# Optimization experiments

Measured on AMD Instinct MI355X. Metric: run time of the kernel, lower is better.

Reference implementation:

```python
import jax, jax.numpy as jnp
import numpy as np

N, E, F_IN, HID, HEADS, OUT = 50000, 800000, 128, 64, 4, 40


def gat_layer(x, src, dst, n, W, a_src, a_dst, b, heads, ch):
    # PyG GATConv: h = x @ W per head; e_ij = LeakyReLU(a_src.h_j + a_dst.h_i)
    h = (x @ W).reshape(n, heads, ch)
    al_s = jnp.einsum('nhc,hc->nh', h, a_src)  # source-side logit term
    al_d = jnp.einsum('nhc,hc->nh', h, a_dst)  # target-side logit term
    e = jax.nn.leaky_relu(al_s[src] + al_d[dst], negative_slope=0.2)  # [E,H]
    m = jax.ops.segment_max(e, dst, num_segments=n)  # stable softmax per target node
    e = jnp.exp(e - m[dst])
    s = jax.ops.segment_sum(e, dst, num_segments=n)
    alpha = e / s[dst]  # [E,H]
    out = jax.ops.segment_sum(h[src] * alpha[:, :, None], dst, num_segments=n)  # [n,H,C]
    return out.reshape(n, heads * ch) + b


def gat_forward(x, src, dst, W0, as0, ad0, b0, W1, as1, ad1, b1, W2, as2, ad2, b2):
    n = x.shape[0]
    x = jax.nn.elu(gat_layer(x, src, dst, n, W0, as0, ad0, b0, HEADS, HID))
    x = jax.nn.elu(gat_layer(x, src, dst, n, W1, as1, ad1, b1, HEADS, HID))
    x = gat_layer(x, src, dst, n, W2, as2, ad2, b2, 1, OUT)
    return jax.nn.log_softmax(x, axis=1)


def setup_inputs() -> dict:
    key = jax.random.key(0)
    ks = jax.random.split(key, 16)
    x = jax.random.normal(ks[0], (N, F_IN), dtype=jnp.float32)
    edge_index = jax.random.randint(ks[1], (2, E), 0, N, dtype=jnp.int64)
    g = lambda k, sh: jax.random.normal(k, sh, dtype=jnp.float32) * (1.0 / np.sqrt(sh[0]))
    d_hid = HID * HEADS
    return {
        'x': x, 'edge_index': edge_index,
        'W0': g(ks[2], (F_IN, d_hid)), 'as0': g(ks[3], (HEADS, HID)), 'ad0': g(ks[4], (HEADS, HID)), 'b0': jnp.zeros((d_hid,), jnp.float32),
        'W1': g(ks[5], (d_hid, d_hid)), 'as1': g(ks[6], (HEADS, HID)), 'ad1': g(ks[7], (HEADS, HID)), 'b1': jnp.zeros((d_hid,), jnp.float32),
        'W2': g(ks[8], (d_hid, OUT)), 'as2': g(ks[9], (1, OUT)), 'ad2': g(ks[10], (1, OUT)), 'b2': jnp.zeros((OUT,), jnp.float32),
    }


def reference(x, edge_index, W0, as0, ad0, b0, W1, as1, ad1, b1, W2, as2, ad2, b2):
    n = x.shape[0]
    loops = jnp.arange(n, dtype=edge_index.dtype)  # PyG add_self_loops=True
    src = jnp.concatenate([edge_index[0], loops])
    dst = jnp.concatenate([edge_index[1], loops])
    return gat_forward(x, src, dst, W0, as0, ad0, b0, W1, as1, ad1, b1, W2, as2, ad2, b2)
```

## Files before the change

kernel.cpp:

```cpp
#include <hip/hip_runtime.h>
#include <math.h>

#define NODES 50000
#define NEDGES 800000
#define TOT_E (NEDGES + NODES)
#define SCAN_B 256
#define SCAN_NB ((NODES + SCAN_B - 1) / SCAN_B)

typedef __attribute__((ext_vector_type(8))) short short8v;
typedef __attribute__((ext_vector_type(4))) float f32x4;

static __device__ __forceinline__ float lrelu(float z) {
  return z > 0.f ? z : 0.2f * z;
}
static __device__ __forceinline__ float b2f(ushort u) {
  union { uint i; float f; } v; v.i = ((uint)u) << 16; return v.f;
}
static __device__ __forceinline__ ushort f2b(float f) {
  union { float f; uint i; } v; v.f = f;
  uint r = v.i + 0x7fff + ((v.i >> 16) & 1);
  return (ushort)(r >> 16);
}

__global__ void k_hist(const int* __restrict__ dst, int* __restrict__ counts) {
  int stride = gridDim.x * blockDim.x;
  for (int i = blockIdx.x * blockDim.x + threadIdx.x; i < TOT_E; i += stride) {
    int d = (i < NEDGES) ? dst[i] : (i - NEDGES);
    atomicAdd(&counts[d], 1);
  }
}

__global__ __launch_bounds__(SCAN_B) void k_scan_red(const int* __restrict__ counts,
                                                     int* __restrict__ bsum) {
  __shared__ int sm[SCAN_B];
  int idx = blockIdx.x * SCAN_B + threadIdx.x;
  int v = (idx < NODES) ? counts[idx] : 0;
  sm[threadIdx.x] = v;
  __syncthreads();
  for (int off = SCAN_B / 2; off > 0; off >>= 1) {
    if (threadIdx.x < off) sm[threadIdx.x] += sm[threadIdx.x + off];
    __syncthreads();
  }
  if (threadIdx.x == 0) bsum[blockIdx.x] = sm[0];
}

__global__ __launch_bounds__(256) void k_scan_part(const int* __restrict__ bsum,
                                                   int* __restrict__ bpre) {
  __shared__ int sm[256];
  int tid = threadIdx.x;
  int v = (tid < SCAN_NB) ? bsum[tid] : 0;
  sm[tid] = v;
  __syncthreads();
  for (int off = 1; off < 256; off <<= 1) {
    int t = (tid >= off) ? sm[tid - off] : 0;
    __syncthreads();
    sm[tid] += t;
    __syncthreads();
  }
  if (tid < SCAN_NB) bpre[tid] = sm[tid] - v;
}

__global__ __launch_bounds__(SCAN_B) void k_scan_emit(const int* __restrict__ counts,
    const int* __restrict__ bpre, int* __restrict__ offs, int* __restrict__ cur) {
  __shared__ int sm[SCAN_B];
  int idx = blockIdx.x * SCAN_B + threadIdx.x;
  int tid = threadIdx.x;
  int v = (idx < NODES) ? counts[idx] : 0;
  sm[tid] = v;
  __syncthreads();
  for (int off = 1; off < SCAN_B; off <<= 1) {
    int t = (tid >= off) ? sm[tid - off] : 0;
    __syncthreads();
    sm[tid] += t;
    __syncthreads();
  }
  int base = bpre[blockIdx.x];
  int excl = base + sm[tid] - v;
  if (idx < NODES) { offs[idx] = excl; cur[idx] = excl; }
  if (idx == NODES - 1) offs[NODES] = excl + v;
}

__global__ void k_scatter(const int* __restrict__ src, const int* __restrict__ dst,
                          int* __restrict__ cur, int* __restrict__ ssrc) {
  int stride = gridDim.x * blockDim.x;
  for (int i = blockIdx.x * blockDim.x + threadIdx.x; i < TOT_E; i += stride) {
    int s, d;
    if (i < NEDGES) { s = src[i]; d = dst[i]; } else { s = i - NEDGES; d = s; }
    int pos = atomicAdd(&cur[d], 1);
    ssrc[pos] = s;
  }
}

__global__ void k_cast4(const float* __restrict__ X, ushort* __restrict__ Xb, int total4) {
  int stride = gridDim.x * blockDim.x;
  for (int i = blockIdx.x * blockDim.x + threadIdx.x; i < total4; i += stride) {
    float4 v = *(const float4*)&X[i * 4];
    ushort4 o;
    o.x = f2b(v.x); o.y = f2b(v.y); o.z = f2b(v.z); o.w = f2b(v.w);
    *(ushort4*)&Xb[i * 4] = o;
  }
}

__global__ void k_packB(const float* __restrict__ W, ushort* __restrict__ Bp,
                        int N, int NF, int total) {
  int idx = blockIdx.x * blockDim.x + threadIdx.x;
  if (idx >= total) return;
  int i = idx & 7;
  int lane = (idx >> 3) & 63;
  int rem = idx >> 9;
  int nf = rem % NF;
  int kf = rem / NF;
  int k = kf * 32 + (lane >> 4) * 8 + i;
  int col = nf * 16 + (lane & 15);
  float v = (col < N) ? W[(size_t)k * N + col] : 0.f;
  Bp[idx] = f2b(v);
}

template<int KF, int NFW, int CG, int HEADS, int NF_TOT>
__global__ __launch_bounds__(256, 2) void k_gemm_reg(
    const ushort* __restrict__ A, const ushort* __restrict__ Bp,
    ushort* __restrict__ H, const float* __restrict__ a_s, const float* __restrict__ a_d,
    float* __restrict__ al_s, float* __restrict__ al_d, int M, int N, int K) {
  int wave = (blockIdx.x * blockDim.x + threadIdx.x) >> 6;
  int lane = threadIdx.x & 63;
  int lg = lane >> 4;
  int lr = lane & 15;
  int total_waves = (gridDim.x * blockDim.x) >> 6;
  int wpc = total_waves / CG;
  int cg = wave / wpc;
  int mslot = wave - cg * wpc;
  if (cg >= CG) return;

  short8v b[KF][NFW];
#pragma unroll
  for (int kf = 0; kf < KF; ++kf)
#pragma unroll
    for (int n = 0; n < NFW; ++n)
      b[kf][n] = *(const short8v*)(Bp + ((size_t)(kf * NF_TOT + cg * NFW + n) * 64 + lane) * 8);

  float asc[NFW], adc[NFW];
#pragma unroll
  for (int n = 0; n < NFW; ++n) {
    int col = (cg * NFW + n) * 16 + lr;
    bool ok = col < N;
    asc[n] = ok ? a_s[col] : 0.f;
    adc[n] = ok ? a_d[col] : 0.f;
  }

  int nstrips = M >> 4;
  for (int strip = mslot; strip < nstrips; strip += wpc) {
    const ushort* arow = A + (size_t)(strip * 16 + lr) * K + lg * 8;
    short8v a[KF];
#pragma unroll
    for (int kf = 0; kf < KF; ++kf) a[kf] = *(const short8v*)(arow + kf * 32);
    f32x4 acc[NFW];
#pragma unroll
    for (int n = 0; n < NFW; ++n) acc[n] = (f32x4){0.f, 0.f, 0.f, 0.f};
#pragma unroll
    for (int kf = 0; kf < KF; ++kf)
#pragma unroll
      for (int n = 0; n < NFW; ++n)
        acc[n] = __builtin_amdgcn_mfma_f32_16x16x32_bf16(a[kf], b[kf][n], acc[n], 0, 0, 0);

#pragma unroll
    for (int n = 0; n < NFW; ++n) {
      int col = (cg * NFW + n) * 16 + lr;
      if (col < N) {
#pragma unroll
        for (int r = 0; r < 4; ++r) {
          int row = strip * 16 + lg * 4 + r;
          H[(size_t)row * N + col] = f2b(acc[n][r]);
        }
      }
    }

    float ps[4], pd[4];
#pragma unroll
    for (int r = 0; r < 4; ++r) {
      float s = 0.f, d = 0.f;
#pragma unroll
      for (int n = 0; n < NFW; ++n) {
        s += acc[n][r] * asc[n];
        d += acc[n][r] * adc[n];
      }
      ps[r] = s; pd[r] = d;
    }
#pragma unroll
    for (int off = 1; off <= 8; off <<= 1)
#pragma unroll
      for (int t = 0; t < 4; ++t) {
        ps[t] += __shfl_xor(ps[t], off);
        pd[t] += __shfl_xor(pd[t], off);
      }
    if (lr < 4) {
      int row = strip * 16 + lg * 4 + lr;
      if (HEADS == 4) {
        al_s[row * 4 + cg] = ps[lr];
        al_d[row * 4 + cg] = pd[lr];
      } else {
        al_s[row] = ps[lr];
        al_d[row] = pd[lr];
      }
    }
  }
}

__global__ __launch_bounds__(256) void k_agg4(const ushort* __restrict__ hb,
    const float* __restrict__ al_s, const float* __restrict__ al_d,
    const int* __restrict__ offs, const int* __restrict__ ssrc,
    const float* __restrict__ bias, ushort* __restrict__ outb) {
  int wid = (blockIdx.x * blockDim.x + threadIdx.x) >> 6;
  if (wid >= NODES) return;
  int lane = threadIdx.x & 63;
  int beg = offs[wid], end = offs[wid + 1];
  float4 ald4 = *(const float4*)&al_d[wid * 4];

  float m[4], s[4];
#pragma unroll
  for (int h = 0; h < 4; ++h) { m[h] = -1e30f; s[h] = 0.f; }
  for (int i = beg + lane; i < end; i += 64) {
    int sv = ssrc[i];
    float4 a4 = *(const float4*)&al_s[sv * 4];
    float z0 = lrelu(a4.x + ald4.x), z1 = lrelu(a4.y + ald4.y);
    float z2 = lrelu(a4.z + ald4.z), z3 = lrelu(a4.w + ald4.w);
    float z[4] = {z0, z1, z2, z3};
#pragma unroll
    for (int h = 0; h < 4; ++h) {
      if (z[h] > m[h]) { s[h] = s[h] * __expf(m[h] - z[h]) + 1.f; m[h] = z[h]; }
      else s[h] += __expf(z[h] - m[h]);
    }
  }
#pragma unroll
  for (int off = 1; off <= 32; off <<= 1) {
#pragma unroll
    for (int h = 0; h < 4; ++h) {
      float mo = __shfl_xor(m[h], off), so = __shfl_xor(s[h], off);
      float mn = fmaxf(m[h], mo);
      s[h] = s[h] * __expf(m[h] - mn) + so * __expf(mo - mn);
      m[h] = mn;
    }
  }
  float inv[4];
#pragma unroll
  for (int h = 0; h < 4; ++h) inv[h] = 1.f / s[h];

  int q = lane >> 4;
  int c = lane & 15;
  int hsel = c >> 2;
  float facc[16];
#pragma unroll
  for (int j = 0; j < 16; ++j) facc[j] = 0.f;

  for (int cb = beg; cb < end; cb += 64) {
    int cnt = min(64, end - cb);
    float av0 = 0.f, av1 = 0.f, av2 = 0.f, av3 = 0.f;
    int myidx = 0;
    if (lane < cnt) {
      myidx = ssrc[cb + lane];
      float4 a4 = *(const float4*)&al_s[myidx * 4];
      av0 = __expf(lrelu(a4.x + ald4.x) - m[0]) * inv[0];
      av1 = __expf(lrelu(a4.y + ald4.y) - m[1]) * inv[1];
      av2 = __expf(lrelu(a4.z + ald4.z) - m[2]) * inv[2];
      av3 = __expf(lrelu(a4.w + ald4.w) - m[3]) * inv[3];
    }
    for (int e = 0; e < cnt; e += 4) {
      int eq = e + q;
      int sv = __shfl(myidx, eq);
      float a0 = __shfl(av0, eq), a1 = __shfl(av1, eq);
      float a2 = __shfl(av2, eq), a3 = __shfl(av3, eq);
      float al = hsel == 0 ? a0 : (hsel == 1 ? a1 : (hsel == 2 ? a2 : a3));
      if (eq < cnt) {
        const ushort* hr = hb + (size_t)sv * 256 + c * 16;
        short8v v0 = *(const short8v*)hr;
        short8v v1 = *(const short8v*)(hr + 8);
#pragma unroll
        for (int j = 0; j < 8; ++j) facc[j] += al * b2f((ushort)v0[j]);
#pragma unroll
        for (int j = 0; j < 8; ++j) facc[j + 8] += al * b2f((ushort)v1[j]);
      }
    }
  }
#pragma unroll
  for (int j = 0; j < 16; ++j) {
    facc[j] += __shfl_xor(facc[j], 16);
    facc[j] += __shfl_xor(facc[j], 32);
  }
  if (q == 0) {
    short8v o0, o1;
#pragma unroll
    for (int j = 0; j < 8; ++j) {
      float v = facc[j] + bias[c * 16 + j];
      o0[j] = (short)f2b(v > 0.f ? v : __expf(v) - 1.f);
      float w = facc[j + 8] + bias[c * 16 + 8 + j];
      o1[j] = (short)f2b(w > 0.f ? w : __expf(w) - 1.f);
    }
    *(short8v*)(outb + (size_t)wid * 256 + c * 16) = o0;
    *(short8v*)(outb + (size_t)wid * 256 + c * 16 + 8) = o1;
  }
}

__global__ __launch_bounds__(256) void k_agg1(const ushort* __restrict__ hb,
    const float* __restrict__ al_s, const float* __restrict__ al_d,
    const int* __restrict__ offs, const int* __restrict__ ssrc,
    const float* __restrict__ bias, float* __restrict__ out) {
  int wid = (blockIdx.x * blockDim.x + threadIdx.x) >> 6;
  if (wid >= NODES) return;
  int lane = threadIdx.x & 63;
  int beg = offs[wid], end = offs[wid + 1];
  float ald = al_d[wid];

  float m = -1e30f, s = 0.f;
  for (int i = beg + lane; i < end; i += 64) {
    float z = lrelu(al_s[ssrc[i]] + ald);
    if (z > m) { s = s * __expf(m - z) + 1.f; m = z; }
    else s += __expf(z - m);
  }
#pragma unroll
  for (int off = 1; off <= 32; off <<= 1) {
    float mo = __shfl_xor(m, off), so = __shfl_xor(s, off);
    float mn = fmaxf(m, mo);
    s = s * __expf(m - mn) + so * __expf(mo - mn);
    m = mn;
  }
  float inv = 1.f / s;

  int q = lane >> 4;
  int cq = lane & 15;
  bool act = cq < 10;
  float acc[4] = {0.f, 0.f, 0.f, 0.f};
  for (int cb = beg; cb < end; cb += 64) {
    int cnt = min(64, end - cb);
    float av = 0.f;
    int myidx = 0;
    if (lane < cnt) {
      myidx = ssrc[cb + lane];
      av = __expf(lrelu(al_s[myidx] + ald) - m) * inv;
    }
    for (int e = 0; e < cnt; e += 4) {
      int eq = e + q;
      int sv = __shfl(myidx, eq);
      float al = __shfl(av, eq);
      if (eq < cnt && act) {
        ushort4 hv = *(const ushort4*)&hb[(size_t)sv * 40 + cq * 4];
        acc[0] += al * b2f(hv.x); acc[1] += al * b2f(hv.y);
        acc[2] += al * b2f(hv.z); acc[3] += al * b2f(hv.w);
      }
    }
  }
#pragma unroll
  for (int j = 0; j < 4; ++j) {
    acc[j] += __shfl_xor(acc[j], 16);
    acc[j] += __shfl_xor(acc[j], 32);
  }
  float v[4];
  float mm = -1e30f;
  if (act) {
#pragma unroll
    for (int j = 0; j < 4; ++j) {
      v[j] = acc[j] + bias[cq * 4 + j];
      mm = fmaxf(mm, v[j]);
    }
  }
#pragma unroll
  for (int off = 1; off <= 8; off <<= 1) mm = fmaxf(mm, __shfl_xor(mm, off));
  float se = 0.f;
  if (act) {
#pragma unroll
    for (int j = 0; j < 4; ++j) se += __expf(v[j] - mm);
  }
#pragma unroll
  for (int off = 1; off <= 8; off <<= 1) se += __shfl_xor(se, off);
  if (act && q == 0) {
    float lse = mm + __logf(se);
    float4 o;
    o.x = v[0] - lse; o.y = v[1] - lse; o.z = v[2] - lse; o.w = v[3] - lse;
    *(float4*)&out[(size_t)wid * 40 + cq * 4] = o;
  }
}

extern "C" void kernel_launch(void* const* d_in, const int* in_sizes, int n_in,
                              void* d_out, int out_size, void* d_ws, size_t ws_size,
                              hipStream_t stream) {
  const float* x   = (const float*)d_in[0];
  const int*   ei  = (const int*)d_in[1];
  const float* W0  = (const float*)d_in[2];
  const float* as0 = (const float*)d_in[3];
  const float* ad0 = (const float*)d_in[4];
  const float* b0  = (const float*)d_in[5];
  const float* W1  = (const float*)d_in[6];
  const float* as1 = (const float*)d_in[7];
  const float* ad1 = (const float*)d_in[8];
  const float* b1  = (const float*)d_in[9];
  const float* W2  = (const float*)d_in[10];
  const float* as2 = (const float*)d_in[11];
  const float* ad2 = (const float*)d_in[12];
  const float* b2  = (const float*)d_in[13];
  float* out = (float*)d_out;

  char* p = (char*)d_ws;
  auto take = [&](size_t bytes) {
    char* q = p;
    p += (bytes + 255) & ~(size_t)255;
    return (void*)q;
  };
  ushort* xb0 = (ushort*)take((size_t)NODES * 128 * 2);
  ushort* xb1 = (ushort*)take((size_t)NODES * 256 * 2);
  ushort* xb2 = (ushort*)take((size_t)NODES * 256 * 2);
  ushort* hb  = (ushort*)take((size_t)NODES * 256 * 2);
  float* als  = (float*)take((size_t)NODES * 4 * 4);
  float* ald  = (float*)take((size_t)NODES * 4 * 4);
  int* ssrc   = (int*)take((size_t)TOT_E * 4);
  int* offs   = (int*)take((size_t)(NODES + 1) * 4);
  int* cur    = (int*)take((size_t)NODES * 4);
  int* cnt    = (int*)take((size_t)NODES * 4);
  int* bsum   = (int*)take((size_t)SCAN_NB * 4);
  int* bpre   = (int*)take((size_t)SCAN_NB * 4);
  ushort* Bp0 = (ushort*)take((size_t)4 * 16 * 512 * 2);
  ushort* Bp1 = (ushort*)take((size_t)8 * 16 * 512 * 2);
  ushort* Bp2 = (ushort*)take((size_t)8 * 3 * 512 * 2);

  hipMemsetAsync(cnt, 0, (size_t)NODES * 4, stream);
  k_hist<<<2048, 256, 0, stream>>>(ei + NEDGES, cnt);
  k_scan_red<<<SCAN_NB, SCAN_B, 0, stream>>>(cnt, bsum);
  k_scan_part<<<1, 256, 0, stream>>>(bsum, bpre);
  k_scan_emit<<<SCAN_NB, SCAN_B, 0, stream>>>(cnt, bpre, offs, cur);
  k_scatter<<<2048, 256, 0, stream>>>(ei, ei + NEDGES, cur, ssrc);

  k_cast4<<<2048, 256, 0, stream>>>(x, xb0, NODES * 128 / 4);
  {
    int t0 = 4 * 16 * 512;  k_packB<<<(t0 + 255) / 256, 256, 0, stream>>>(W0, Bp0, 256, 16, t0);
    int t1 = 8 * 16 * 512;  k_packB<<<(t1 + 255) / 256, 256, 0, stream>>>(W1, Bp1, 256, 16, t1);
    int t2 = 8 * 3 * 512;   k_packB<<<(t2 + 255) / 256, 256, 0, stream>>>(W2, Bp2, 40, 3, t2);
  }

  int nwb = (NODES * 64 + 255) / 256;
  int ggb = 512;

  k_gemm_reg<4, 4, 4, 4, 16><<<ggb, 256, 0, stream>>>(xb0, Bp0, hb, as0, ad0, als, ald, NODES, 256, 128);
  k_agg4<<<nwb, 256, 0, stream>>>(hb, als, ald, offs, ssrc, b0, xb1);

  k_gemm_reg<8, 4, 4, 4, 16><<<ggb, 256, 0, stream>>>(xb1, Bp1, hb, as1, ad1, als, ald, NODES, 256, 256);
  k_agg4<<<nwb, 256, 0, stream>>>(hb, als, ald, offs, ssrc, b1, xb2);

  k_gemm_reg<8, 3, 1, 1, 3><<<ggb, 256, 0, stream>>>(xb2, Bp2, hb, as2, ad2, als, ald, NODES, 40, 256);
  k_agg1<<<nwb, 256, 0, stream>>>(hb, als, ald, offs, ssrc, b2, out);
}
```

Measured before the change: 356.0 us.

## Stage edge indices and attention weights in LDS and unroll gather loops

The aggregation kernels now store each 64-edge chunk's source indices and normalized attention weights in per-wave shared memory, replacing the per-edge shuffle broadcasts. k_agg4 is remapped so 32 lanes cover a 256-wide bf16 row with one 16-byte load each, two edges per wave step, which cuts the cross-lane reduction to a single xor step. Both kernels unroll the gather loop to keep two row loads in flight. The cost is extra LDS traffic and wave-level fences that stall until LDS operations finish.

```diff
diff --git a/kernel.cpp b/kernel.cpp
--- a/kernel.cpp
+++ b/kernel.cpp
@@ -20,6 +20,11 @@
   union { float f; uint i; } v; v.f = f;
   uint r = v.i + 0x7fff + ((v.i >> 16) & 1);
   return (ushort)(r >> 16);
+}
+static __device__ __forceinline__ void wave_lds_fence() {
+  __builtin_amdgcn_wave_barrier();
+  asm volatile("s_waitcnt lgkmcnt(0)" ::: "memory");
+  __builtin_amdgcn_sched_barrier(0);
 }
 
 __global__ void k_hist(const int* __restrict__ dst, int* __restrict__ counts) {
@@ -209,6 +214,9 @@
     const float* __restrict__ al_s, const float* __restrict__ al_d,
     const int* __restrict__ offs, const int* __restrict__ ssrc,
     const float* __restrict__ bias, ushort* __restrict__ outb) {
+  __shared__ int s_idx[4][64];
+  __shared__ float s_al[4][256];
+  int w = threadIdx.x >> 6;
   int wid = (blockIdx.x * blockDim.x + threadIdx.x) >> 6;
   if (wid >= NODES) return;
   int lane = threadIdx.x & 63;
@@ -221,9 +229,8 @@
   for (int i = beg + lane; i < end; i += 64) {
     int sv = ssrc[i];
     float4 a4 = *(const float4*)&al_s[sv * 4];
-    float z0 = lrelu(a4.x + ald4.x), z1 = lrelu(a4.y + ald4.y);
-    float z2 = lrelu(a4.z + ald4.z), z3 = lrelu(a4.w + ald4.w);
-    float z[4] = {z0, z1, z2, z3};
+    float z[4] = {lrelu(a4.x + ald4.x), lrelu(a4.y + ald4.y),
+                  lrelu(a4.z + ald4.z), lrelu(a4.w + ald4.w)};
 #pragma unroll
     for (int h = 0; h < 4; ++h) {
       if (z[h] > m[h]) { s[h] = s[h] * __expf(m[h] - z[h]) + 1.f; m[h] = z[h]; }
@@ -244,58 +251,56 @@
 #pragma unroll
   for (int h = 0; h < 4; ++h) inv[h] = 1.f / s[h];
 
-  int q = lane >> 4;
-  int c = lane & 15;
-  int hsel = c >> 2;
-  float facc[16];
-#pragma unroll
-  for (int j = 0; j < 16; ++j) facc[j] = 0.f;
+  int half = lane >> 5;
+  int cl = lane & 31;
+  int hh = cl >> 3;
+  float facc[8] = {0.f, 0.f, 0.f, 0.f, 0.f, 0.f, 0.f, 0.f};
 
   for (int cb = beg; cb < end; cb += 64) {
     int cnt = min(64, end - cb);
-    float av0 = 0.f, av1 = 0.f, av2 = 0.f, av3 = 0.f;
-    int myidx = 0;
+    wave_lds_fence();
     if (lane < cnt) {
-      myidx = ssrc[cb + lane];
-      float4 a4 = *(const float4*)&al_s[myidx * 4];
-      av0 = __expf(lrelu(a4.x + ald4.x) - m[0]) * inv[0];
-      av1 = __expf(lrelu(a4.y + ald4.y) - m[1]) * inv[1];
-      av2 = __expf(lrelu(a4.z + ald4.z) - m[2]) * inv[2];
-      av3 = __expf(lrelu(a4.w + ald4.w) - m[3]) * inv[3];
-    }
-    for (int e = 0; e < cnt; e += 4) {
-      int eq = e + q;
-      int sv = __shfl(myidx, eq);
-      float a0 = __shfl(av0, eq), a1 = __shfl(av1, eq);
-      float a2 = __shfl(av2, eq), a3 = __shfl(av3, eq);
-      float al = hsel == 0 ? a0 : (hsel == 1 ? a1 : (hsel == 2 ? a2 : a3));
-      if (eq < cnt) {
-        const ushort* hr = hb + (size_t)sv * 256 + c * 16;
-        short8v v0 = *(const short8v*)hr;
-        short8v v1 = *(const short8v*)(hr + 8);
-#pragma unroll
-        for (int j = 0; j < 8; ++j) facc[j] += al * b2f((ushort)v0[j]);
-#pragma unroll
-        for (int j = 0; j < 8; ++j) facc[j + 8] += al * b2f((ushort)v1[j]);
-      }
-    }
-  }
-#pragma unroll
-  for (int j = 0; j < 16; ++j) {
-    facc[j] += __shfl_xor(facc[j], 16);
-    facc[j] += __shfl_xor(facc[j], 32);
-  }
-  if (q == 0) {
-    short8v o0, o1;
+      int sv = ssrc[cb + lane];
+      float4 a4 = *(const float4*)&al_s[sv * 4];
+      float4 al;
+      al.x = __expf(lrelu(a4.x + ald4.x) - m[0]) * inv[0];
+      al.y = __expf(lrelu(a4.y + ald4.y) - m[1]) * inv[1];
+      al.z = __expf(lrelu(a4.z + ald4.z) - m[2]) * inv[2];
+      al.w = __expf(lrelu(a4.w + ald4.w) - m[3]) * inv[3];
+      s_idx[w][lane] = sv;
+      *(float4*)&s_al[w][lane * 4] = al;
+    }
+    wave_lds_fence();
+    int e = half;
+    for (; e + 2 < cnt; e += 4) {
+      int sv0 = s_idx[w][e], sv1 = s_idx[w][e + 2];
+      float a0 = s_al[w][e * 4 + hh];
+      float a1 = s_al[w][(e + 2) * 4 + hh];
+      short8v hv0 = *(const short8v*)(hb + (size_t)sv0 * 256 + cl * 8);
+      short8v hv1 = *(const short8v*)(hb + (size_t)sv1 * 256 + cl * 8);
+#pragma unroll
+      for (int j = 0; j < 8; ++j) facc[j] += a0 * b2f((ushort)hv0[j]);
+#pragma unroll
+      for (int j = 0; j < 8; ++j) facc[j] += a1 * b2f((ushort)hv1[j]);
+    }
+    for (; e < cnt; e += 2) {
+      int sv = s_idx[w][e];
+      float al = s_al[w][e * 4 + hh];
+      short8v hv = *(const short8v*)(hb + (size_t)sv * 256 + cl * 8);
+#pragma unroll
+      for (int j = 0; j < 8; ++j) facc[j] += al * b2f((ushort)hv[j]);
+    }
+  }
+#pragma unroll
+  for (int j = 0; j < 8; ++j) facc[j] += __shfl_xor(facc[j], 32);
+  if (half == 0) {
+    short8v o;
 #pragma unroll
     for (int j = 0; j < 8; ++j) {
-      float v = facc[j] + bias[c * 16 + j];
-      o0[j] = (short)f2b(v > 0.f ? v : __expf(v) - 1.f);
-      float w = facc[j + 8] + bias[c * 16 + 8 + j];
-      o1[j] = (short)f2b(w > 0.f ? w : __expf(w) - 1.f);
-    }
-    *(short8v*)(outb + (size_t)wid * 256 + c * 16) = o0;
-    *(short8v*)(outb + (size_t)wid * 256 + c * 16 + 8) = o1;
+      float v = facc[j] + bias[cl * 8 + j];
+      o[j] = (short)f2b(v > 0.f ? v : __expf(v) - 1.f);
+    }
+    *(short8v*)(outb + (size_t)wid * 256 + cl * 8) = o;
   }
 }
 
@@ -303,6 +308,9 @@
     const float* __restrict__ al_s, const float* __restrict__ al_d,
     const int* __restrict__ offs, const int* __restrict__ ssrc,
     const float* __restrict__ bias, float* __restrict__ out) {
+  __shared__ int s_idx[4][64];
+  __shared__ float s_al[4][64];
+  int w = threadIdx.x >> 6;
   int wid = (blockIdx.x * blockDim.x + threadIdx.x) >> 6;
   if (wid >= NODES) return;
   int lane = threadIdx.x & 63;
@@ -330,17 +338,30 @@
   float acc[4] = {0.f, 0.f, 0.f, 0.f};
   for (int cb = beg; cb < end; cb += 64) {
     int cnt = min(64, end - cb);
-    float av = 0.f;
-    int myidx = 0;
+    wave_lds_fence();
     if (lane < cnt) {
-      myidx = ssrc[cb + lane];
-      av = __expf(lrelu(al_s[myidx] + ald) - m) * inv;
-    }
-    for (int e = 0; e < cnt; e += 4) {
-      int eq = e + q;
-      int sv = __shfl(myidx, eq);
-      float al = __shfl(av, eq);
-      if (eq < cnt && act) {
+      int sv = ssrc[cb + lane];
+      s_idx[w][lane] = sv;
+      s_al[w][lane] = __expf(lrelu(al_s[sv] + ald) - m) * inv;
+    }
+    wave_lds_fence();
+    int e = q;
+    for (; e + 4 < cnt; e += 8) {
+      int sv0 = s_idx[w][e], sv1 = s_idx[w][e + 4];
+      float a0 = s_al[w][e], a1 = s_al[w][e + 4];
+      if (act) {
+        ushort4 hv0 = *(const ushort4*)&hb[(size_t)sv0 * 40 + cq * 4];
+        ushort4 hv1 = *(const ushort4*)&hb[(size_t)sv1 * 40 + cq * 4];
+        acc[0] += a0 * b2f(hv0.x) + a1 * b2f(hv1.x);
+        acc[1] += a0 * b2f(hv0.y) + a1 * b2f(hv1.y);
+        acc[2] += a0 * b2f(hv0.z) + a1 * b2f(hv1.z);
+        acc[3] += a0 * b2f(hv0.w) + a1 * b2f(hv1.w);
+      }
+    }
+    for (; e < cnt; e += 4) {
+      int sv = s_idx[w][e];
+      float al = s_al[w][e];
+      if (act) {
         ushort4 hv = *(const ushort4*)&hb[(size_t)sv * 40 + cq * 4];
         acc[0] += al * b2f(hv.x); acc[1] += al * b2f(hv.y);
         acc[2] += al * b2f(hv.z); acc[3] += al * b2f(hv.w);
```

After: 331.4 us. 6.9% less time.
